# Kernel tuning notes

Measured on AMD Instinct MI355X. Metric: run time of the kernel, lower is better.

## Reference

```python
import jax, jax.numpy as jnp
import numpy as np

B, L, CIN, H, K = 32, 4096, 128, 256, 3


def setup_inputs() -> dict:
    key = jax.random.key(0)
    k1, k2, k3 = jax.random.split(key, 3)
    x = jax.random.normal(k1, (B, L, CIN), dtype=jnp.float32)
    # Conv1d weight: (out_ch=3H, in_ch=CIN, kernel=K), fan-in scaled like torch default
    W = jax.random.normal(k2, (3 * H, CIN, K), dtype=jnp.float32) * (1.0 / np.sqrt(CIN * K))
    b = jax.random.normal(k3, (3 * H,), dtype=jnp.float32) * 0.01
    return {"x": x, "W": W, "b": b}


def reference(x, W, b):
    # x: (B, L, CIN) -> (B, CIN, L), matching torch's x.transpose(1, 2)
    xc = jnp.transpose(x, (0, 2, 1))
    # valid 1D conv -> (B, 3H, T) with T = L - K + 1
    conv = jax.lax.conv_general_dilated(
        xc, W, window_strides=(1,), padding="VALID",
        dimension_numbers=("NCH", "OIH", "NCH"),
    ) + b[None, :, None]
    Z, F, O = jnp.split(conv, 3, axis=1)
    Z = jnp.tanh(Z)
    F = jax.nn.sigmoid(F)
    O = jax.nn.sigmoid(O)
    # sequential fo-pool: h_t = O_t * (F_t * h_{t-1} + (1 - F_t) * Z_t)
    zs = jnp.moveaxis(Z, 2, 0)   # (T, B, H)
    fs = jnp.moveaxis(F, 2, 0)
    os_ = jnp.moveaxis(O, 2, 0)
    h0 = jnp.zeros((x.shape[0], H), dtype=Z.dtype)

    def step(h, zfo):
        z, f, o = zfo
        h = o * (f * h + (1.0 - f) * z)
        return h, None

    hT, _ = jax.lax.scan(step, h0, (zs, fs, os_))
    return hT  # (B, H): final hidden state
```

## Files before the change

### kernel.cpp

```cpp
#include <hip/hip_runtime.h>
#include <math.h>

#define B_    32
#define L_    4096
#define CIN_  128
#define H_    256
#define T_    4094
#define KTOT_ 384

#define MT_   128
#define NTB_  32
#define NG_   192
#define NKT_  12

typedef float f32x4 __attribute__((ext_vector_type(4)));
typedef short s16x8 __attribute__((ext_vector_type(8)));

static __device__ __forceinline__ unsigned short f2bf(float f) {
  unsigned u = __builtin_bit_cast(unsigned, f);
  u = (u + 0x7FFFu + ((u >> 16) & 1u)) >> 16;
  return (unsigned short)u;
}

__global__ __launch_bounds__(256) void packW_bf16(const float* __restrict__ W,
                                                  unsigned short* __restrict__ Wb) {
  const int tidg = blockIdx.x * 256 + threadIdx.x;
  const int c = tidg % NG_;
  int t = tidg / NG_;
  const int kgrp = t & 3;  t >>= 2;
  const int kt = t % NKT_;
  const int g = t / NKT_;
  const int q = c >> 4, lr = c & 15;
  const int gate = q % 3, hgrp = q / 3;
  const int hl = hgrp * 16 + lr;
  const int oc = gate * 256 + g * 64 + hl;
  s16x8 outv;
#pragma unroll
  for (int e = 0; e < 8; ++e) {
    const int kk = kt * 32 + kgrp * 8 + e;
    const int i = kk & 127, k = kk >> 7;
    outv[e] = (short)f2bf(W[(size_t)oc * KTOT_ + i * 3 + k]);
  }
  *(s16x8*)(Wb + (size_t)tidg * 8) = outv;
}

__global__ __launch_bounds__(512, 4) void conv_scan_mfma(
    const float* __restrict__ x, const unsigned short* __restrict__ Wb,
    const float* __restrict__ bias, float* __restrict__ Pc,
    float* __restrict__ Sc) {
  __shared__ __align__(16) char smem[33280 + 1024];
  char* xs = smem;
  float2* wmbuf = (float2*)(smem + 33280);

  const int tid = threadIdx.x;
  const int w = tid >> 6;
  const int wm = w >> 2;
  const int wn = w & 3;
  const int l = tid & 63;
  const int lr = l & 15;
  const int lg = l >> 4;
  const int bid = blockIdx.x;
  const int g = bid & 3;
  const int r2 = bid >> 2;
  const int bb = r2 & 31;
  const int tblk = r2 >> 5;
  const int t0 = tblk * MT_;

  const unsigned short* bp = Wb + (size_t)g * 73728 + lg * 1536 + (wn * 48 + lr) * 8;

  s16x8 bcur[3];
#pragma unroll
  for (int nj = 0; nj < 3; ++nj)
    bcur[nj] = *(const s16x8*)(bp + nj * 128);

  for (int v = tid; v < 130 * 32; v += 512) {
    const int row = v >> 5;
    const int colb = (v & 31) * 8;
    int r = t0 + row;
    if (r > L_ - 1) r = L_ - 1;
    const float4 xv = *(const float4*)&x[((size_t)bb * L_ + r) * CIN_ + (v & 31) * 4];
    unsigned p0, p1;
    asm("v_cvt_pk_bf16_f32 %0, %1, %2" : "=v"(p0) : "v"(xv.x), "v"(xv.y));
    asm("v_cvt_pk_bf16_f32 %0, %1, %2" : "=v"(p1) : "v"(xv.z), "v"(xv.w));
    *(uint2*)(xs + row * 256 + (colb ^ ((row & 7) << 4))) = make_uint2(p0, p1);
  }

  f32x4 acc[4][3];
#pragma unroll
  for (int mi = 0; mi < 4; ++mi)
#pragma unroll
    for (int nj = 0; nj < 3; ++nj) acc[mi][nj] = (f32x4)0.f;

  __syncthreads();

#pragma unroll
  for (int kt = 0; kt < NKT_; ++kt) {
    s16x8 bnxt[3];
    if (kt < NKT_ - 1) {
#pragma unroll
      for (int nj = 0; nj < 3; ++nj)
        bnxt[nj] = *(const s16x8*)(bp + (kt + 1) * 6144 + nj * 128);
    }
    const int kof = kt >> 2;
    const int cb = (kt & 3) * 64 + lg * 16;
    s16x8 a[4];
#pragma unroll
    for (int mi = 0; mi < 4; ++mi) {
      const int row = wm * 64 + mi * 16 + lr + kof;
      a[mi] = *(const s16x8*)(xs + row * 256 + (cb ^ ((row & 7) << 4)));
    }
#pragma unroll
    for (int mi = 0; mi < 4; ++mi)
#pragma unroll
      for (int nj = 0; nj < 3; ++nj)
        acc[mi][nj] = __builtin_amdgcn_mfma_f32_16x16x32_bf16(a[mi], bcur[nj], acc[mi][nj], 0, 0, 0);
    if (kt < NKT_ - 1) {
#pragma unroll
      for (int nj = 0; nj < 3; ++nj) bcur[nj] = bnxt[nj];
    }
  }

  const int hl = wn * 16 + lr;
  const float bz = bias[g * 64 + hl];
  const float bf_ = bias[256 + g * 64 + hl];
  const float bo_ = bias[512 + g * 64 + hl];

  float Pw = 1.f, Sw = 0.f;
#pragma unroll
  for (int mi = 0; mi < 4; ++mi) {
    float Pr = 1.f, Sr = 0.f;
#pragma unroll
    for (int r = 0; r < 4; ++r) {
      const int t = t0 + wm * 64 + mi * 16 + lg * 4 + r;
      const float zr = acc[mi][0][r] + bz;
      const float fr = acc[mi][1][r] + bf_;
      const float orr = acc[mi][2][r] + bo_;
      const float zc = fminf(fmaxf(zr, -15.f), 15.f);
      const float e2 = __expf(2.f * zc);
      const float zt = (e2 - 1.f) * __builtin_amdgcn_rcpf(e2 + 1.f);
      const float ft = __builtin_amdgcn_rcpf(1.f + __expf(-fr));
      const float ot = __builtin_amdgcn_rcpf(1.f + __expf(-orr));
      float A = ot * ft;
      float Bv = ot * (1.f - ft) * zt;
      const bool valid = (t < T_);
      A = valid ? A : 1.f;
      Bv = valid ? Bv : 0.f;
      Sr = A * Sr + Bv;
      Pr = A * Pr;
    }
    float Pp = __shfl_xor(Pr, 16), Sp = __shfl_xor(Sr, 16);
    if (lg & 1) { Sr = Pr * Sp + Sr; Pr = Pr * Pp; }
    else        { Sr = Pp * Sr + Sp; Pr = Pp * Pr; }
    Pp = __shfl_xor(Pr, 32); Sp = __shfl_xor(Sr, 32);
    if (lg & 2) { Sr = Pr * Sp + Sr; Pr = Pr * Pp; }
    else        { Sr = Pp * Sr + Sp; Pr = Pp * Pr; }
    Sw = Pr * Sw + Sr;
    Pw = Pr * Pw;
  }

  if (lg == 0) wmbuf[wm * 64 + hl] = make_float2(Pw, Sw);
  __syncthreads();
  if (tid < 64) {
    const float2 e0 = wmbuf[tid];
    const float2 e1 = wmbuf[64 + tid];
    const float P = e1.x * e0.x;
    const float S = e1.x * e0.y + e1.y;
    const size_t o = ((size_t)bb * NTB_ + tblk) * H_ + g * 64 + tid;
    Pc[o] = P;
    Sc[o] = S;
  }
}

__global__ __launch_bounds__(128) void combine_kernel(const float* __restrict__ Pc,
                                                      const float* __restrict__ Sc,
                                                      float* __restrict__ out) {
  const int idx = blockIdx.x * 128 + threadIdx.x;
  const int b = idx >> 8;
  const int h = idx & 255;
  float hv = 0.f;
#pragma unroll 8
  for (int c = 0; c < NTB_; ++c) {
    const float p = Pc[((size_t)b * NTB_ + c) * H_ + h];
    const float s = Sc[((size_t)b * NTB_ + c) * H_ + h];
    hv = p * hv + s;
  }
  out[idx] = hv;
}

extern "C" void kernel_launch(void* const* d_in, const int* in_sizes, int n_in,
                              void* d_out, int out_size, void* d_ws, size_t ws_size,
                              hipStream_t stream) {
  const float* x = (const float*)d_in[0];
  const float* W = (const float*)d_in[1];
  const float* bias = (const float*)d_in[2];
  float* out = (float*)d_out;

  char* ws = (char*)d_ws;
  unsigned short* Wb = (unsigned short*)ws;
  float* Pc = (float*)(ws + (1 << 20));
  float* Sc = (float*)(ws + 2 * (1 << 20));

  packW_bf16<<<144, 256, 0, stream>>>(W, Wb);
  conv_scan_mfma<<<4096, 512, 0, stream>>>(x, Wb, bias, Pc, Sc);
  combine_kernel<<<64, 128, 0, stream>>>(Pc, Sc, out);
}
```

Before: 193.9 us.

## Cover all hidden channels per block with 64-step time tiles

Each block now covers all 256 hidden channels (16 waves of 1024 threads) for a 64-step time tile, where before four channel-group blocks each handled 128 steps. Each x tile is therefore loaded and converted to bf16 once rather than four times, and the cross-wave LDS combine and its barrier go away. In exchange, time chunks double, so the combine pass has twice as many sequential steps. The 1024-thread blocks with min 4 blocks per CU also squeeze the register budget, which could cause spills.

```diff
diff --git a/kernel.cpp b/kernel.cpp
--- a/kernel.cpp
+++ b/kernel.cpp
@@ -8,9 +8,8 @@
 #define T_    4094
 #define KTOT_ 384
 
-#define MT_   128
-#define NTB_  32
-#define NG_   192
+#define MT_   64
+#define NTB_  64
 #define NKT_  12
 
 typedef float f32x4 __attribute__((ext_vector_type(4)));
@@ -24,16 +23,14 @@
 
 __global__ __launch_bounds__(256) void packW_bf16(const float* __restrict__ W,
                                                   unsigned short* __restrict__ Wb) {
-  const int tidg = blockIdx.x * 256 + threadIdx.x;
-  const int c = tidg % NG_;
-  int t = tidg / NG_;
-  const int kgrp = t & 3;  t >>= 2;
-  const int kt = t % NKT_;
-  const int g = t / NKT_;
+  const int idx = blockIdx.x * 256 + threadIdx.x;
+  const int c = idx % 768;
+  const int t = idx / 768;
+  const int kgrp = t & 3;
+  const int kt = t >> 2;
   const int q = c >> 4, lr = c & 15;
   const int gate = q % 3, hgrp = q / 3;
-  const int hl = hgrp * 16 + lr;
-  const int oc = gate * 256 + g * 64 + hl;
+  const int oc = gate * 256 + hgrp * 16 + lr;
   s16x8 outv;
 #pragma unroll
   for (int e = 0; e < 8; ++e) {
@@ -41,39 +38,33 @@
     const int i = kk & 127, k = kk >> 7;
     outv[e] = (short)f2bf(W[(size_t)oc * KTOT_ + i * 3 + k]);
   }
-  *(s16x8*)(Wb + (size_t)tidg * 8) = outv;
+  *(s16x8*)(Wb + (size_t)idx * 8) = outv;
 }
 
-__global__ __launch_bounds__(512, 4) void conv_scan_mfma(
+__global__ __launch_bounds__(1024, 4) void conv_scan_mfma(
     const float* __restrict__ x, const unsigned short* __restrict__ Wb,
     const float* __restrict__ bias, float* __restrict__ Pc,
     float* __restrict__ Sc) {
-  __shared__ __align__(16) char smem[33280 + 1024];
-  char* xs = smem;
-  float2* wmbuf = (float2*)(smem + 33280);
+  __shared__ __align__(16) char xs[66 * 256];
 
   const int tid = threadIdx.x;
-  const int w = tid >> 6;
-  const int wm = w >> 2;
-  const int wn = w & 3;
+  const int wn = tid >> 6;
   const int l = tid & 63;
   const int lr = l & 15;
   const int lg = l >> 4;
   const int bid = blockIdx.x;
-  const int g = bid & 3;
-  const int r2 = bid >> 2;
-  const int bb = r2 & 31;
-  const int tblk = r2 >> 5;
+  const int bb = bid & 31;
+  const int tblk = bid >> 5;
   const int t0 = tblk * MT_;
 
-  const unsigned short* bp = Wb + (size_t)g * 73728 + lg * 1536 + (wn * 48 + lr) * 8;
+  const unsigned short* bp = Wb + lg * 6144 + (wn * 48 + lr) * 8;
 
   s16x8 bcur[3];
 #pragma unroll
   for (int nj = 0; nj < 3; ++nj)
     bcur[nj] = *(const s16x8*)(bp + nj * 128);
 
-  for (int v = tid; v < 130 * 32; v += 512) {
+  for (int v = tid; v < 66 * 32; v += 1024) {
     const int row = v >> 5;
     const int colb = (v & 31) * 8;
     int r = t0 + row;
@@ -99,14 +90,14 @@
     if (kt < NKT_ - 1) {
 #pragma unroll
       for (int nj = 0; nj < 3; ++nj)
-        bnxt[nj] = *(const s16x8*)(bp + (kt + 1) * 6144 + nj * 128);
+        bnxt[nj] = *(const s16x8*)(bp + (kt + 1) * 24576 + nj * 128);
     }
     const int kof = kt >> 2;
     const int cb = (kt & 3) * 64 + lg * 16;
     s16x8 a[4];
 #pragma unroll
     for (int mi = 0; mi < 4; ++mi) {
-      const int row = wm * 64 + mi * 16 + lr + kof;
+      const int row = mi * 16 + lr + kof;
       a[mi] = *(const s16x8*)(xs + row * 256 + (cb ^ ((row & 7) << 4)));
     }
 #pragma unroll
@@ -121,9 +112,9 @@
   }
 
   const int hl = wn * 16 + lr;
-  const float bz = bias[g * 64 + hl];
-  const float bf_ = bias[256 + g * 64 + hl];
-  const float bo_ = bias[512 + g * 64 + hl];
+  const float bz = bias[hl];
+  const float bf_ = bias[256 + hl];
+  const float bo_ = bias[512 + hl];
 
   float Pw = 1.f, Sw = 0.f;
 #pragma unroll
@@ -131,7 +122,7 @@
     float Pr = 1.f, Sr = 0.f;
 #pragma unroll
     for (int r = 0; r < 4; ++r) {
-      const int t = t0 + wm * 64 + mi * 16 + lg * 4 + r;
+      const int t = t0 + mi * 16 + lg * 4 + r;
       const float zr = acc[mi][0][r] + bz;
       const float fr = acc[mi][1][r] + bf_;
       const float orr = acc[mi][2][r] + bo_;
@@ -158,16 +149,10 @@
     Pw = Pr * Pw;
   }
 
-  if (lg == 0) wmbuf[wm * 64 + hl] = make_float2(Pw, Sw);
-  __syncthreads();
-  if (tid < 64) {
-    const float2 e0 = wmbuf[tid];
-    const float2 e1 = wmbuf[64 + tid];
-    const float P = e1.x * e0.x;
-    const float S = e1.x * e0.y + e1.y;
-    const size_t o = ((size_t)bb * NTB_ + tblk) * H_ + g * 64 + tid;
-    Pc[o] = P;
-    Sc[o] = S;
+  if (lg == 0) {
+    const size_t o = ((size_t)bb * NTB_ + tblk) * H_ + hl;
+    Pc[o] = Pw;
+    Sc[o] = Sw;
   }
 }
 
@@ -198,9 +183,9 @@
   char* ws = (char*)d_ws;
   unsigned short* Wb = (unsigned short*)ws;
   float* Pc = (float*)(ws + (1 << 20));
-  float* Sc = (float*)(ws + 2 * (1 << 20));
+  float* Sc = (float*)(ws + 3 * (1 << 20));
 
   packW_bf16<<<144, 256, 0, stream>>>(W, Wb);
-  conv_scan_mfma<<<4096, 512, 0, stream>>>(x, Wb, bias, Pc, Sc);
+  conv_scan_mfma<<<2048, 1024, 0, stream>>>(x, Wb, bias, Pc, Sc);
   combine_kernel<<<64, 128, 0, stream>>>(Pc, Sc, out);
 }
```

New measurement: 182.9 us. 1.06x faster.
